# Kernel optimization log

Hardware: AMD Instinct MI355X
Metric: run time of the kernel (lower is better)

The kernel has to match this reference:

```python
import jax, jax.numpy as jnp
import numpy as np

H = 1024   # context_size == review_len (code requires equality)
B = 64     # batch_size
T = 1024   # review_len


def setup_inputs() -> dict:
    key = jax.random.key(0)
    k1, k2 = jax.random.split(key)
    decoder_hidden = jax.random.normal(k1, (B, H), dtype=jnp.float32)
    # original indexes encoder_outputs[:, batch, t] -> vector of size H
    encoder_outputs = jax.random.normal(k2, (H, B, T), dtype=jnp.float32)
    return {"decoder_hidden": decoder_hidden, "encoder_outputs": encoder_outputs}


def reference(decoder_hidden, encoder_outputs):
    # score[b,t] = dot(decoder_hidden[b], encoder_outputs[:, b, t])  ('dot' method)
    scores = jnp.einsum('hbt,bh->bt', encoder_outputs, decoder_hidden)  # [B,T]
    # weighted[h,b,t] = encoder_outputs[h,b,t] * score[b,t]
    weighted = encoder_outputs * scores[None, :, :]                      # [H,B,T]
    # per t: softmax over hidden dim of the [B,H] matrix, then sum over t
    sm = jax.nn.softmax(weighted, axis=0)                                # softmax over H
    attn_energies = jnp.sum(sm, axis=2).T                                # [B,H] (== [B, review_len])
    return attn_energies
```

## Files before the change

kernel.cpp:

```cpp
#include <hip/hip_runtime.h>
#include <math.h>

#define H  1024
#define B  64
#define T  1024
#define BT (B*T)
#define TC 32
#define SPLIT 8
#define CHUNKS 4
#define NT 512

__device__ __forceinline__ float ex2(float x) { return __builtin_amdgcn_exp2f(x); }

__global__ __launch_bounds__(NT)
__attribute__((amdgpu_waves_per_eu(4)))
void attn_main(const float* __restrict__ dec,
               const float* __restrict__ enc,
               float* __restrict__ ws)
{
    __shared__ float rbuf[3][8][TC];
    __shared__ float prm[2][TC];

    const int tid   = threadIdx.x;
    const int split = blockIdx.x;
    const int b     = blockIdx.y;
    const int lane  = tid & 63;
    const int wave  = tid >> 6;
    const int r     = tid >> 3;
    const int c8    = tid & 7;

    const float L2E = 1.44269504088896340736f;

    float acc[16];
    #pragma unroll
    for (int i = 0; i < 16; ++i) acc[i] = 0.f;

    for (int c = 0; c < CHUNKS; ++c) {
        const int t0 = (split * CHUNKS + c) * TC;

        float4 v[16];
        float4 s4  = make_float4(0.f, 0.f, 0.f, 0.f);
        float4 mx4 = make_float4(-INFINITY, -INFINITY, -INFINITY, -INFINITY);
        float4 mn4 = make_float4( INFINITY,  INFINITY,  INFINITY,  INFINITY);
        #pragma unroll
        for (int i = 0; i < 16; ++i) {
            const int h = r + 64*i;
            v[i] = *reinterpret_cast<const float4*>(enc + (size_t)h*BT + b*T + t0 + 4*c8);
            const float dh = dec[b*H + h];
            s4.x = fmaf(v[i].x, dh, s4.x); s4.y = fmaf(v[i].y, dh, s4.y);
            s4.z = fmaf(v[i].z, dh, s4.z); s4.w = fmaf(v[i].w, dh, s4.w);
            mx4.x = fmaxf(mx4.x, v[i].x); mx4.y = fmaxf(mx4.y, v[i].y);
            mx4.z = fmaxf(mx4.z, v[i].z); mx4.w = fmaxf(mx4.w, v[i].w);
            mn4.x = fminf(mn4.x, v[i].x); mn4.y = fminf(mn4.y, v[i].y);
            mn4.z = fminf(mn4.z, v[i].z); mn4.w = fminf(mn4.w, v[i].w);
        }
        #pragma unroll
        for (int off = 8; off <= 32; off <<= 1) {
            s4.x += __shfl_xor(s4.x, off); s4.y += __shfl_xor(s4.y, off);
            s4.z += __shfl_xor(s4.z, off); s4.w += __shfl_xor(s4.w, off);
            mx4.x = fmaxf(mx4.x, __shfl_xor(mx4.x, off)); mx4.y = fmaxf(mx4.y, __shfl_xor(mx4.y, off));
            mx4.z = fmaxf(mx4.z, __shfl_xor(mx4.z, off)); mx4.w = fmaxf(mx4.w, __shfl_xor(mx4.w, off));
            mn4.x = fminf(mn4.x, __shfl_xor(mn4.x, off)); mn4.y = fminf(mn4.y, __shfl_xor(mn4.y, off));
            mn4.z = fminf(mn4.z, __shfl_xor(mn4.z, off)); mn4.w = fminf(mn4.w, __shfl_xor(mn4.w, off));
        }
        if (lane < 8) {
            *reinterpret_cast<float4*>(&rbuf[0][wave][lane*4]) = s4;
            *reinterpret_cast<float4*>(&rbuf[1][wave][lane*4]) = mx4;
            *reinterpret_cast<float4*>(&rbuf[2][wave][lane*4]) = mn4;
        }
        __syncthreads();
        if (tid < TC) {
            float s  = rbuf[0][0][tid];
            float mx = rbuf[1][0][tid];
            float mn = rbuf[2][0][tid];
            #pragma unroll
            for (int w = 1; w < 8; ++w) {
                s += rbuf[0][w][tid];
                mx = fmaxf(mx, rbuf[1][w][tid]);
                mn = fminf(mn, rbuf[2][w][tid]);
            }
            const float m = (s >= 0.f) ? s*mx : s*mn;
            prm[0][tid] = s * L2E;
            prm[1][tid] = m * L2E;
        }
        __syncthreads();

        {
            const float4 sv = *reinterpret_cast<const float4*>(&prm[0][c8*4]);
            const float4 mv = *reinterpret_cast<const float4*>(&prm[1][c8*4]);
            float4 d4 = make_float4(0.f, 0.f, 0.f, 0.f);
            #pragma unroll
            for (int i = 0; i < 16; ++i) {
                v[i].x = ex2(fmaf(v[i].x, sv.x, -mv.x));
                v[i].y = ex2(fmaf(v[i].y, sv.y, -mv.y));
                v[i].z = ex2(fmaf(v[i].z, sv.z, -mv.z));
                v[i].w = ex2(fmaf(v[i].w, sv.w, -mv.w));
                d4.x += v[i].x; d4.y += v[i].y; d4.z += v[i].z; d4.w += v[i].w;
            }
            #pragma unroll
            for (int off = 8; off <= 32; off <<= 1) {
                d4.x += __shfl_xor(d4.x, off); d4.y += __shfl_xor(d4.y, off);
                d4.z += __shfl_xor(d4.z, off); d4.w += __shfl_xor(d4.w, off);
            }
            if (lane < 8)
                *reinterpret_cast<float4*>(&rbuf[0][wave][lane*4]) = d4;
        }
        __syncthreads();
        if (tid < TC) {
            float d = rbuf[0][0][tid];
            #pragma unroll
            for (int w = 1; w < 8; ++w) d += rbuf[0][w][tid];
            prm[0][tid] = 1.0f / d;
        }
        __syncthreads();

        {
            const float4 rv = *reinterpret_cast<const float4*>(&prm[0][c8*4]);
            #pragma unroll
            for (int i = 0; i < 16; ++i) {
                acc[i] = fmaf(v[i].x, rv.x, acc[i]);
                acc[i] = fmaf(v[i].y, rv.y, acc[i]);
                acc[i] = fmaf(v[i].z, rv.z, acc[i]);
                acc[i] = fmaf(v[i].w, rv.w, acc[i]);
            }
        }
        __syncthreads();
    }

    #pragma unroll
    for (int i = 0; i < 16; ++i) {
        acc[i] += __shfl_xor(acc[i], 1);
        acc[i] += __shfl_xor(acc[i], 2);
        acc[i] += __shfl_xor(acc[i], 4);
    }
    const size_t wbase = (size_t)(b * SPLIT + split) * H;
    #pragma unroll
    for (int i = 0; i < 16; ++i) {
        if ((i >> 1) == c8)
            ws[wbase + r + 64*i] = acc[i];
    }
}

__global__ __launch_bounds__(256) void attn_reduce(const float* __restrict__ ws,
                                                   float* __restrict__ out)
{
    const int idx = blockIdx.x * 256 + threadIdx.x;
    const int b = idx >> 10;
    const int h = idx & 1023;
    float s = 0.f;
    #pragma unroll
    for (int sp = 0; sp < SPLIT; ++sp)
        s += ws[(size_t)(b * SPLIT + sp) * H + h];
    out[idx] = s;
}

extern "C" void kernel_launch(void* const* d_in, const int* in_sizes, int n_in,
                              void* d_out, int out_size, void* d_ws, size_t ws_size,
                              hipStream_t stream)
{
    const float* dec = (const float*)d_in[0];
    const float* enc = (const float*)d_in[1];
    float* out = (float*)d_out;
    float* ws  = (float*)d_ws;

    attn_main  <<<dim3(SPLIT, B), NT, 0, stream>>>(dec, enc, ws);
    attn_reduce<<<dim3((B*H)/256), 256, 0, stream>>>(ws, out);
}
```

Before: 376.9 us.

## Prefetch next encoder chunk into LDS via async global_load_lds during compute

Stages each 1024x32 encoder chunk into a 128KB LDS buffer with global_load_lds. After the current chunk is copied into registers, the load for the next chunk is issued so the global fetch overlaps the softmax math. It also hoists the decoder vector into registers, halves the split count while doubling the chunks per block, and swaps __syncthreads for explicit waitcnt barriers. The large LDS footprint limits occupancy to one block per CU, and the grid shrinks to 256 blocks, so parallelism drops in exchange for the overlap.

Result: no change. 384.1 us (+1.9%).

```diff
diff --git a/kernel.cpp b/kernel.cpp
--- a/kernel.cpp
+++ b/kernel.cpp
@@ -6,18 +6,26 @@
 #define T  1024
 #define BT (B*T)
 #define TC 32
-#define SPLIT 8
-#define CHUNKS 4
+#define SPLIT 4
+#define CHUNKS 8
 #define NT 512
 
+typedef __attribute__((address_space(1))) unsigned int* gp_t;
+typedef __attribute__((address_space(3))) unsigned int* lp_t;
+
 __device__ __forceinline__ float ex2(float x) { return __builtin_amdgcn_exp2f(x); }
 
+#define BAR_LGKM() do { asm volatile("s_waitcnt lgkmcnt(0)" ::: "memory"); \
+                        __builtin_amdgcn_s_barrier(); } while (0)
+#define BAR_ALL()  do { asm volatile("s_waitcnt vmcnt(0) lgkmcnt(0)" ::: "memory"); \
+                        __builtin_amdgcn_s_barrier(); } while (0)
+
 __global__ __launch_bounds__(NT)
-__attribute__((amdgpu_waves_per_eu(4)))
 void attn_main(const float* __restrict__ dec,
                const float* __restrict__ enc,
                float* __restrict__ ws)
 {
+    __shared__ float buf[H * TC];
     __shared__ float rbuf[3][8][TC];
     __shared__ float prm[2][TC];
 
@@ -28,27 +36,55 @@
     const int wave  = tid >> 6;
     const int r     = tid >> 3;
     const int c8    = tid & 7;
+    const int lr    = lane >> 3;
+    const int lc    = lane & 7;
 
     const float L2E = 1.44269504088896340736f;
 
+    float dh[16];
+    #pragma unroll
+    for (int i = 0; i < 16; ++i) dh[i] = dec[b*H + r + 64*i];
+
     float acc[16];
     #pragma unroll
     for (int i = 0; i < 16; ++i) acc[i] = 0.f;
 
+    {
+        const int t0 = split * CHUNKS * TC;
+        #pragma unroll
+        for (int j = 0; j < 16; ++j) {
+            const int row0 = (wave*16 + j) * 8;
+            const float* g = enc + (size_t)(row0 + lr)*BT + b*T + t0 + lc*4;
+            __builtin_amdgcn_global_load_lds((gp_t)g, (lp_t)&buf[row0*TC], 16, 0, 0);
+        }
+    }
+    BAR_ALL();
+
     for (int c = 0; c < CHUNKS; ++c) {
-        const int t0 = (split * CHUNKS + c) * TC;
-
         float4 v[16];
+        #pragma unroll
+        for (int i = 0; i < 16; ++i)
+            v[i] = *reinterpret_cast<const float4*>(&buf[(r + 64*i)*TC + c8*4]);
+        BAR_LGKM();
+        __builtin_amdgcn_sched_barrier(0);
+
+        if (c + 1 < CHUNKS) {
+            const int t0n = (split*CHUNKS + c + 1) * TC;
+            #pragma unroll
+            for (int j = 0; j < 16; ++j) {
+                const int row0 = (wave*16 + j) * 8;
+                const float* g = enc + (size_t)(row0 + lr)*BT + b*T + t0n + lc*4;
+                __builtin_amdgcn_global_load_lds((gp_t)g, (lp_t)&buf[row0*TC], 16, 0, 0);
+            }
+        }
+
         float4 s4  = make_float4(0.f, 0.f, 0.f, 0.f);
         float4 mx4 = make_float4(-INFINITY, -INFINITY, -INFINITY, -INFINITY);
         float4 mn4 = make_float4( INFINITY,  INFINITY,  INFINITY,  INFINITY);
         #pragma unroll
         for (int i = 0; i < 16; ++i) {
-            const int h = r + 64*i;
-            v[i] = *reinterpret_cast<const float4*>(enc + (size_t)h*BT + b*T + t0 + 4*c8);
-            const float dh = dec[b*H + h];
-            s4.x = fmaf(v[i].x, dh, s4.x); s4.y = fmaf(v[i].y, dh, s4.y);
-            s4.z = fmaf(v[i].z, dh, s4.z); s4.w = fmaf(v[i].w, dh, s4.w);
+            s4.x = fmaf(v[i].x, dh[i], s4.x); s4.y = fmaf(v[i].y, dh[i], s4.y);
+            s4.z = fmaf(v[i].z, dh[i], s4.z); s4.w = fmaf(v[i].w, dh[i], s4.w);
             mx4.x = fmaxf(mx4.x, v[i].x); mx4.y = fmaxf(mx4.y, v[i].y);
             mx4.z = fmaxf(mx4.z, v[i].z); mx4.w = fmaxf(mx4.w, v[i].w);
             mn4.x = fminf(mn4.x, v[i].x); mn4.y = fminf(mn4.y, v[i].y);
@@ -68,7 +104,7 @@
             *reinterpret_cast<float4*>(&rbuf[1][wave][lane*4]) = mx4;
             *reinterpret_cast<float4*>(&rbuf[2][wave][lane*4]) = mn4;
         }
-        __syncthreads();
+        BAR_LGKM();
         if (tid < TC) {
             float s  = rbuf[0][0][tid];
             float mx = rbuf[1][0][tid];
@@ -83,7 +119,7 @@
             prm[0][tid] = s * L2E;
             prm[1][tid] = m * L2E;
         }
-        __syncthreads();
+        BAR_LGKM();
 
         {
             const float4 sv = *reinterpret_cast<const float4*>(&prm[0][c8*4]);
@@ -105,14 +141,14 @@
             if (lane < 8)
                 *reinterpret_cast<float4*>(&rbuf[0][wave][lane*4]) = d4;
         }
-        __syncthreads();
+        BAR_LGKM();
         if (tid < TC) {
             float d = rbuf[0][0][tid];
             #pragma unroll
             for (int w = 1; w < 8; ++w) d += rbuf[0][w][tid];
             prm[0][tid] = 1.0f / d;
         }
-        __syncthreads();
+        BAR_LGKM();
 
         {
             const float4 rv = *reinterpret_cast<const float4*>(&prm[0][c8*4]);
@@ -124,7 +160,8 @@
                 acc[i] = fmaf(v[i].w, rv.w, acc[i]);
             }
         }
-        __syncthreads();
+        BAR_ALL();
+        __builtin_amdgcn_sched_barrier(0);
     }
 
     #pragma unroll
```

## Double-buffer encoder tiles via async global-to-LDS loads and per-wave column softmax

Applied to the files above, without the earlier changes.

Encoder tiles are now staged into a double-buffered LDS area with global_load_lds, with XOR swizzling, and explicit vmcnt waits and barriers so the next chunk's loads overlap compute. After the transpose each wave owns whole t-columns, so the softmax sum, max, min and denominator reductions run entirely with wave shuffles instead of cross-wave LDS reductions and __syncthreads. Each wave writes its own partial row, which makes the reduce kernel sum 32 partials per output instead of 8. The split count drops from 8 to 4 with twice as many chunks, which halves the block count and raises the workspace traffic.

Result: no change. 377.9 us (+0.3%).

```diff
diff --git a/kernel.cpp b/kernel.cpp
--- a/kernel.cpp
+++ b/kernel.cpp
@@ -6,56 +6,99 @@
 #define T  1024
 #define BT (B*T)
 #define TC 32
-#define SPLIT 8
-#define CHUNKS 4
+#define SPLIT 4
+#define CHUNKS 8
 #define NT 512
+#define HROWS 512
+
+typedef __attribute__((address_space(1))) unsigned int* gp_t;
+typedef __attribute__((address_space(3))) unsigned int* lp_t;
 
 __device__ __forceinline__ float ex2(float x) { return __builtin_amdgcn_exp2f(x); }
 
+#define WAITV8() asm volatile("s_waitcnt vmcnt(8)" ::: "memory")
+#define WAITV0() asm volatile("s_waitcnt vmcnt(0)" ::: "memory")
+#define WAITL0() asm volatile("s_waitcnt lgkmcnt(0)" ::: "memory")
+#define BAR()    __builtin_amdgcn_s_barrier()
+
+#define STAGE(bi, hb, tcol0) do {                                            \
+    _Pragma("unroll")                                                        \
+    for (int j = 0; j < 8; ++j) {                                            \
+        const int lrow = wave*64 + j*8;                                      \
+        const float* g = enc + (size_t)((hb)*HROWS + lrow + lr)*BT           \
+                             + b*T + (tcol0) + 4*(lc ^ lr);                  \
+        __builtin_amdgcn_global_load_lds((gp_t)g,                            \
+            (lp_t)&buf[bi][lrow*TC], 16, 0, 0);                              \
+    }                                                                        \
+} while (0)
+
 __global__ __launch_bounds__(NT)
-__attribute__((amdgpu_waves_per_eu(4)))
 void attn_main(const float* __restrict__ dec,
                const float* __restrict__ enc,
                float* __restrict__ ws)
 {
-    __shared__ float rbuf[3][8][TC];
-    __shared__ float prm[2][TC];
+    __shared__ float buf[2][HROWS * TC];
 
     const int tid   = threadIdx.x;
     const int split = blockIdx.x;
     const int b     = blockIdx.y;
     const int lane  = tid & 63;
     const int wave  = tid >> 6;
-    const int r     = tid >> 3;
-    const int c8    = tid & 7;
+    const int lr    = lane >> 3;
+    const int lc    = lane & 7;
 
     const float L2E = 1.44269504088896340736f;
+    const int   t0  = split * CHUNKS * TC;
+
+    const float* rd0 = &buf[0][lane*TC + (wave ^ (lane & 7))*4];
+    const float* rd1 = &buf[1][lane*TC + (wave ^ (lane & 7))*4];
+
+    float dh[16];
+    #pragma unroll
+    for (int i = 0; i < 16; ++i) dh[i] = dec[b*H + lane + 64*i];
 
     float acc[16];
     #pragma unroll
     for (int i = 0; i < 16; ++i) acc[i] = 0.f;
 
+    STAGE(0, 0, t0);
+    STAGE(1, 1, t0);
+
+    #pragma unroll 1
     for (int c = 0; c < CHUNKS; ++c) {
-        const int t0 = (split * CHUNKS + c) * TC;
+        const bool more = (c + 1 < CHUNKS);
+        const int  tn   = t0 + (c + 1) * TC;
 
+        WAITV8();  BAR();
         float4 v[16];
+        #pragma unroll
+        for (int i = 0; i < 8; ++i)
+            v[i] = *reinterpret_cast<const float4*>(rd0 + i*64*TC);
+        WAITL0();  BAR();
+        if (more) STAGE(0, 0, tn);
+
+        if (more) { WAITV8(); } else { WAITV0(); }
+        BAR();
+        #pragma unroll
+        for (int i = 0; i < 8; ++i)
+            v[8+i] = *reinterpret_cast<const float4*>(rd1 + i*64*TC);
+        WAITL0();  BAR();
+        if (more) STAGE(1, 1, tn);
+
         float4 s4  = make_float4(0.f, 0.f, 0.f, 0.f);
         float4 mx4 = make_float4(-INFINITY, -INFINITY, -INFINITY, -INFINITY);
         float4 mn4 = make_float4( INFINITY,  INFINITY,  INFINITY,  INFINITY);
         #pragma unroll
         for (int i = 0; i < 16; ++i) {
-            const int h = r + 64*i;
-            v[i] = *reinterpret_cast<const float4*>(enc + (size_t)h*BT + b*T + t0 + 4*c8);
-            const float dh = dec[b*H + h];
-            s4.x = fmaf(v[i].x, dh, s4.x); s4.y = fmaf(v[i].y, dh, s4.y);
-            s4.z = fmaf(v[i].z, dh, s4.z); s4.w = fmaf(v[i].w, dh, s4.w);
+            s4.x = fmaf(v[i].x, dh[i], s4.x); s4.y = fmaf(v[i].y, dh[i], s4.y);
+            s4.z = fmaf(v[i].z, dh[i], s4.z); s4.w = fmaf(v[i].w, dh[i], s4.w);
             mx4.x = fmaxf(mx4.x, v[i].x); mx4.y = fmaxf(mx4.y, v[i].y);
             mx4.z = fmaxf(mx4.z, v[i].z); mx4.w = fmaxf(mx4.w, v[i].w);
             mn4.x = fminf(mn4.x, v[i].x); mn4.y = fminf(mn4.y, v[i].y);
             mn4.z = fminf(mn4.z, v[i].z); mn4.w = fminf(mn4.w, v[i].w);
         }
         #pragma unroll
-        for (int off = 8; off <= 32; off <<= 1) {
+        for (int off = 1; off <= 32; off <<= 1) {
             s4.x += __shfl_xor(s4.x, off); s4.y += __shfl_xor(s4.y, off);
             s4.z += __shfl_xor(s4.z, off); s4.w += __shfl_xor(s4.w, off);
             mx4.x = fmaxf(mx4.x, __shfl_xor(mx4.x, off)); mx4.y = fmaxf(mx4.y, __shfl_xor(mx4.y, off));
@@ -63,82 +106,41 @@
             mn4.x = fminf(mn4.x, __shfl_xor(mn4.x, off)); mn4.y = fminf(mn4.y, __shfl_xor(mn4.y, off));
             mn4.z = fminf(mn4.z, __shfl_xor(mn4.z, off)); mn4.w = fminf(mn4.w, __shfl_xor(mn4.w, off));
         }
-        if (lane < 8) {
-            *reinterpret_cast<float4*>(&rbuf[0][wave][lane*4]) = s4;
-            *reinterpret_cast<float4*>(&rbuf[1][wave][lane*4]) = mx4;
-            *reinterpret_cast<float4*>(&rbuf[2][wave][lane*4]) = mn4;
+        float4 sl, ml;
+        sl.x = s4.x*L2E; ml.x = ((s4.x >= 0.f) ? s4.x*mx4.x : s4.x*mn4.x)*L2E;
+        sl.y = s4.y*L2E; ml.y = ((s4.y >= 0.f) ? s4.y*mx4.y : s4.y*mn4.y)*L2E;
+        sl.z = s4.z*L2E; ml.z = ((s4.z >= 0.f) ? s4.z*mx4.z : s4.z*mn4.z)*L2E;
+        sl.w = s4.w*L2E; ml.w = ((s4.w >= 0.f) ? s4.w*mx4.w : s4.w*mn4.w)*L2E;
+
+        float4 d4 = make_float4(0.f, 0.f, 0.f, 0.f);
+        #pragma unroll
+        for (int i = 0; i < 16; ++i) {
+            v[i].x = ex2(fmaf(v[i].x, sl.x, -ml.x));
+            v[i].y = ex2(fmaf(v[i].y, sl.y, -ml.y));
+            v[i].z = ex2(fmaf(v[i].z, sl.z, -ml.z));
+            v[i].w = ex2(fmaf(v[i].w, sl.w, -ml.w));
+            d4.x += v[i].x; d4.y += v[i].y; d4.z += v[i].z; d4.w += v[i].w;
         }
-        __syncthreads();
-        if (tid < TC) {
-            float s  = rbuf[0][0][tid];
-            float mx = rbuf[1][0][tid];
-            float mn = rbuf[2][0][tid];
-            #pragma unroll
-            for (int w = 1; w < 8; ++w) {
-                s += rbuf[0][w][tid];
-                mx = fmaxf(mx, rbuf[1][w][tid]);
-                mn = fminf(mn, rbuf[2][w][tid]);
-            }
-            const float m = (s >= 0.f) ? s*mx : s*mn;
-            prm[0][tid] = s * L2E;
-            prm[1][tid] = m * L2E;
+        #pragma unroll
+        for (int off = 1; off <= 32; off <<= 1) {
+            d4.x += __shfl_xor(d4.x, off); d4.y += __shfl_xor(d4.y, off);
+            d4.z += __shfl_xor(d4.z, off); d4.w += __shfl_xor(d4.w, off);
         }
-        __syncthreads();
+        const float4 rv = make_float4(1.0f/d4.x, 1.0f/d4.y, 1.0f/d4.z, 1.0f/d4.w);
 
-        {
-            const float4 sv = *reinterpret_cast<const float4*>(&prm[0][c8*4]);
-            const float4 mv = *reinterpret_cast<const float4*>(&prm[1][c8*4]);
-            float4 d4 = make_float4(0.f, 0.f, 0.f, 0.f);
-            #pragma unroll
-            for (int i = 0; i < 16; ++i) {
-                v[i].x = ex2(fmaf(v[i].x, sv.x, -mv.x));
-                v[i].y = ex2(fmaf(v[i].y, sv.y, -mv.y));
-                v[i].z = ex2(fmaf(v[i].z, sv.z, -mv.z));
-                v[i].w = ex2(fmaf(v[i].w, sv.w, -mv.w));
-                d4.x += v[i].x; d4.y += v[i].y; d4.z += v[i].z; d4.w += v[i].w;
-            }
-            #pragma unroll
-            for (int off = 8; off <= 32; off <<= 1) {
-                d4.x += __shfl_xor(d4.x, off); d4.y += __shfl_xor(d4.y, off);
-                d4.z += __shfl_xor(d4.z, off); d4.w += __shfl_xor(d4.w, off);
-            }
-            if (lane < 8)
-                *reinterpret_cast<float4*>(&rbuf[0][wave][lane*4]) = d4;
+        #pragma unroll
+        for (int i = 0; i < 16; ++i) {
+            acc[i] = fmaf(v[i].x, rv.x, acc[i]);
+            acc[i] = fmaf(v[i].y, rv.y, acc[i]);
+            acc[i] = fmaf(v[i].z, rv.z, acc[i]);
+            acc[i] = fmaf(v[i].w, rv.w, acc[i]);
         }
-        __syncthreads();
-        if (tid < TC) {
-            float d = rbuf[0][0][tid];
-            #pragma unroll
-            for (int w = 1; w < 8; ++w) d += rbuf[0][w][tid];
-            prm[0][tid] = 1.0f / d;
-        }
-        __syncthreads();
-
-        {
-            const float4 rv = *reinterpret_cast<const float4*>(&prm[0][c8*4]);
-            #pragma unroll
-            for (int i = 0; i < 16; ++i) {
-                acc[i] = fmaf(v[i].x, rv.x, acc[i]);
-                acc[i] = fmaf(v[i].y, rv.y, acc[i]);
-                acc[i] = fmaf(v[i].z, rv.z, acc[i]);
-                acc[i] = fmaf(v[i].w, rv.w, acc[i]);
-            }
-        }
-        __syncthreads();
     }
 
+    const size_t wbase = (size_t)((b * SPLIT + split) * 8 + wave) * H;
     #pragma unroll
-    for (int i = 0; i < 16; ++i) {
-        acc[i] += __shfl_xor(acc[i], 1);
-        acc[i] += __shfl_xor(acc[i], 2);
-        acc[i] += __shfl_xor(acc[i], 4);
-    }
-    const size_t wbase = (size_t)(b * SPLIT + split) * H;
-    #pragma unroll
-    for (int i = 0; i < 16; ++i) {
-        if ((i >> 1) == c8)
-            ws[wbase + r + 64*i] = acc[i];
-    }
+    for (int i = 0; i < 16; ++i)
+        ws[wbase + lane + 64*i] = acc[i];
 }
 
 __global__ __launch_bounds__(256) void attn_reduce(const float* __restrict__ ws,
@@ -149,8 +151,8 @@
     const int h = idx & 1023;
     float s = 0.f;
     #pragma unroll
-    for (int sp = 0; sp < SPLIT; ++sp)
-        s += ws[(size_t)(b * SPLIT + sp) * H + h];
+    for (int p = 0; p < SPLIT*8; ++p)
+        s += ws[(size_t)(b * SPLIT*8 + p) * H + h];
     out[idx] = s;
 }
 
```
